# Optimization experiments

Hardware: AMD Instinct MI355X
Metric: run time of the kernel (lower is better)

Reference implementation:

```python
import jax, jax.numpy as jnp
import numpy as np

B, N, C = 8, 4096, 768
H = 4 * C  # mlp hidden
EPS = 1e-7
LN_EPS = 1e-5


def _ln(x, g, b):
    mu = jnp.mean(x, axis=-1, keepdims=True)
    var = jnp.mean((x - mu) ** 2, axis=-1, keepdims=True)
    return (x - mu) * jax.lax.rsqrt(var + LN_EPS) * g + b


def _mlp(z, w1, b1, w2, b2):
    return jax.nn.gelu(z @ w1 + b1, approximate=False) @ w2 + b2


def setup_inputs() -> dict:
    key = jax.random.key(0)
    ks = jax.random.split(key, 16)
    s = 1.0 / np.sqrt(C)
    inp = {
        "x": jax.random.normal(ks[0], (B, N, C), jnp.float32),
        "y": jax.random.normal(ks[1], (B, N, C), jnp.float32),
        "mask": jax.random.randint(ks[2], (B, N, 1), 0, 2).astype(jnp.float32),
        "h": 64,
        "w": 64,
        "ln1_g": jnp.ones((C,), jnp.float32),
        "ln1_b": jnp.zeros((C,), jnp.float32),
        "Wq": jax.random.normal(ks[3], (C, C), jnp.float32) * s,
        "Wk": jax.random.normal(ks[4], (C, C), jnp.float32) * s,
        "Wv": jax.random.normal(ks[5], (C, C), jnp.float32) * s,
        "Wpx": jax.random.normal(ks[6], (2 * C, C), jnp.float32) * s,
        "Wpy": jax.random.normal(ks[7], (2 * C, C), jnp.float32) * s,
        "ln2_g": jnp.ones((C,), jnp.float32),
        "ln2_b": jnp.zeros((C,), jnp.float32),
        "fx1_w": jax.random.normal(ks[8], (C, H), jnp.float32) * s,
        "fx1_b": jnp.zeros((H,), jnp.float32),
        "fx2_w": jax.random.normal(ks[9], (H, C), jnp.float32) / np.sqrt(H),
        "fx2_b": jnp.zeros((C,), jnp.float32),
        "fy1_w": jax.random.normal(ks[10], (C, H), jnp.float32) * s,
        "fy1_b": jnp.zeros((H,), jnp.float32),
        "fy2_w": jax.random.normal(ks[11], (H, C), jnp.float32) / np.sqrt(H),
        "fy2_b": jnp.zeros((C,), jnp.float32),
    }
    return inp


def _minmax(s):
    mn = jnp.min(s, axis=1, keepdims=True)
    mx = jnp.max(s, axis=1, keepdims=True)
    return (s - mn) / (mx - mn + EPS)


def reference(x, y, mask, h, w, ln1_g, ln1_b, Wq, Wk, Wv, Wpx, Wpy,
              ln2_g, ln2_b, fx1_w, fx1_b, fx2_w, fx2_b, fy1_w, fy1_b, fy2_w, fy2_b):
    b, n, c = x.shape
    m = mask.reshape(b, n, 1)  # binary mask per token
    xn = _ln(x, ln1_g, ln1_b)
    yn = _ln(y, ln1_g, ln1_b)
    q = yn @ Wq  # (b,n,c)
    k = xn @ Wk
    v = xn @ Wv
    # masked GAP pools (Weighted_GAP): (b,c)
    fg = jnp.sum(q * m, axis=1) / (jnp.sum(m, axis=1) + 5e-4)
    bg = jnp.sum(q * (1.0 - m), axis=1) / (jnp.sum(1.0 - m, axis=1) + 5e-4)
    k_nrm = jnp.linalg.norm(k, axis=2)  # (b,n)
    fg_nrm = jnp.linalg.norm(fg, axis=1, keepdims=True)  # (b,1)
    bg_nrm = jnp.linalg.norm(bg, axis=1, keepdims=True)
    fg_s = jnp.einsum('bnc,bc->bn', k, fg) / (k_nrm * fg_nrm + EPS)
    bg_s = jnp.einsum('bnc,bc->bn', k, bg) / (k_nrm * bg_nrm + EPS)
    scores = _minmax(fg_s) - _minmax(bg_s)  # (b,n)
    pseudo_mask = scores.reshape(b, 1, h, w)
    attn = jax.nn.softmax(jnp.where(scores < 0, scores - 100.0, scores), axis=1)
    query_pro = jnp.einsum('bn,bnc->bc', attn, v)  # (b,c)
    qp_nrm = jnp.linalg.norm(query_pro, axis=1, keepdims=True)
    sim = jnp.sum(query_pro * fg, axis=1, keepdims=True) / (qp_nrm * fg_nrm + EPS)
    sim = (sim + 1.0) * 0.5  # (b,1)
    pro = sim * fg + (1.0 - sim) * query_pro  # (b,c)
    pro_b = jnp.broadcast_to(pro[:, None, :], x.shape)
    xo = x + jnp.concatenate([x, pro_b], axis=-1) @ Wpx
    yo = y + jnp.concatenate([y, pro_b], axis=-1) @ Wpy
    xo = xo + _mlp(_ln(xo, ln2_g, ln2_b), fx1_w, fx1_b, fx2_w, fx2_b)
    yo = yo + _mlp(_ln(yo, ln2_g, ln2_b), fy1_w, fy1_b, fy2_w, fy2_b)
    return (xo, yo, pseudo_mask)
```

## Files before the change

### kernel.cpp

```cpp
#include <hip/hip_runtime.h>
#include <math.h>

#define B_ 8
#define N_ 4096
#define C_ 768
#define H_ 3072
#define M_ (B_*N_)
#define NSPLIT 16

typedef unsigned short u16;
typedef unsigned int u32;
typedef __attribute__((ext_vector_type(8))) __bf16 bf16x8;
typedef __attribute__((ext_vector_type(4))) float f32x4;
typedef __attribute__((ext_vector_type(4))) unsigned short u16x4;

__device__ __forceinline__ u16 f2bf(float f){
  u32 u = __float_as_uint(f);
  u32 r = (u + 0x7FFFu + ((u >> 16) & 1u)) >> 16;
  return (u16)r;
}
__device__ __forceinline__ float bf2f(u16 h){
  return __uint_as_float(((u32)h) << 16);
}
__device__ __forceinline__ void gload_lds16(const void* g, void* l){
  __builtin_amdgcn_global_load_lds((const __attribute__((address_space(1))) void*)g,
                                   (__attribute__((address_space(3))) void*)l, 16, 0, 0);
}

template<int EPI>
__global__ __launch_bounds__(256) void gemm_bf16(
    const u16* __restrict__ A, const u16* __restrict__ BT,
    int K, int N, int NBN,
    void* __restrict__ outp,
    const float* __restrict__ resid,
    const float* __restrict__ rowv,
    const float* __restrict__ bias)
{
  __shared__ u16 lds[2][8192];
  const int tid = threadIdx.x;
  const int wid = tid >> 6, lane = tid & 63;

  const int nwg = gridDim.x;
  int wg = blockIdx.x;
  wg = (wg & 7) * (nwg >> 3) + (wg >> 3);
  const int GMN = 8 * NBN;
  const int g = wg / GMN, r = wg % GMN;
  const int bm = (g*8 + (r & 7)) * 128;
  const int bn = (r >> 3) * 128;

  const int wr = wid >> 1, wc = wid & 1;

  f32x4 acc[4][4];
#pragma unroll
  for (int i=0;i<4;i++)
#pragma unroll
    for (int j=0;j<4;j++) acc[i][j] = (f32x4){0.f,0.f,0.f,0.f};

  const int idx0 = tid, idx1 = tid + 256;
  const u16* agp0 = A  + (size_t)(bm + (idx0>>2))*K + (idx0&3)*8;
  const u16* agp1 = A  + (size_t)(bm + (idx1>>2))*K + (idx1&3)*8;
  const u16* bgp0 = BT + (size_t)(bn + (idx0>>2))*K + (idx0&3)*8;
  const u16* bgp1 = BT + (size_t)(bn + (idx1>>2))*K + (idx1&3)*8;

  auto STAGE = [&](int c){
    u16* base = lds[c];
    gload_lds16(agp0, base + wid*512);
    gload_lds16(agp1, base + 2048 + wid*512);
    gload_lds16(bgp0, base + 4096 + wid*512);
    gload_lds16(bgp1, base + 6144 + wid*512);
    agp0 += 32; agp1 += 32; bgp0 += 32; bgp1 += 32;
  };

  const int aoff = (wr*64 + (lane&15))*32 + (lane>>4)*8;
  const int boff = 4096 + (wc*64 + (lane&15))*32 + (lane>>4)*8;

  const int nk = K >> 5;
  STAGE(0);
  __syncthreads();
  int cur = 0;
  for (int kk=0; kk<nk; kk++){
    if (kk+1 < nk) STAGE(cur^1);
    bf16x8 av[4], bv[4];
    const u16* pa = &lds[cur][aoff];
    const u16* pb = &lds[cur][boff];
#pragma unroll
    for (int i=0;i<4;i++){
      av[i] = *reinterpret_cast<const bf16x8*>(pa + i*512);
      bv[i] = *reinterpret_cast<const bf16x8*>(pb + i*512);
    }
#pragma unroll
    for (int i=0;i<4;i++)
#pragma unroll
      for (int j=0;j<4;j++)
        acc[i][j] = __builtin_amdgcn_mfma_f32_16x16x32_bf16(av[i], bv[j], acc[i][j], 0, 0, 0);
    __syncthreads();
    cur ^= 1;
  }

  const int col0 = bn + wc*64 + (lane & 15);
  const int row0 = bm + wr*64 + ((lane >> 4) << 2);
#pragma unroll
  for (int i=0;i<4;i++){
#pragma unroll
    for (int j=0;j<4;j++){
#pragma unroll
      for (int r2=0;r2<4;r2++){
        const int row = row0 + i*16 + r2;
        const int cj  = col0 + j*16;
        const size_t o = (size_t)row*N + cj;
        const float va = acc[i][j][r2];
        if constexpr (EPI == 0){
          ((u16*)outp)[o] = f2bf(va);
        } else if constexpr (EPI == 1){
          ((float*)outp)[o] = resid[o] + va + rowv[(row >> 12)*N + cj];
        } else if constexpr (EPI == 2){
          const float z = va + bias[cj];
          ((u16*)outp)[o] = f2bf(0.5f*z*(1.0f + erff(z*0.70710678f)));
        } else {
          float* po = (float*)outp + o;
          *po += va + bias[cj];
        }
      }
    }
  }
}

__global__ __launch_bounds__(256) void ln_fwd(const float* __restrict__ in,
    const float* __restrict__ gam, const float* __restrict__ bet,
    u16* __restrict__ out)
{
  const int row  = blockIdx.x*4 + (threadIdx.x >> 6);
  const int lane = threadIdx.x & 63;
  const float* p = in + (size_t)row * C_;
  float4 v0 = *reinterpret_cast<const float4*>(p + lane*4);
  float4 v1 = *reinterpret_cast<const float4*>(p + lane*4 + 256);
  float4 v2 = *reinterpret_cast<const float4*>(p + lane*4 + 512);
  float s  = v0.x+v0.y+v0.z+v0.w + v1.x+v1.y+v1.z+v1.w + v2.x+v2.y+v2.z+v2.w;
  float sq = v0.x*v0.x+v0.y*v0.y+v0.z*v0.z+v0.w*v0.w
           + v1.x*v1.x+v1.y*v1.y+v1.z*v1.z+v1.w*v1.w
           + v2.x*v2.x+v2.y*v2.y+v2.z*v2.z+v2.w*v2.w;
#pragma unroll
  for (int o=32;o>0;o>>=1){ s += __shfl_xor(s,o); sq += __shfl_xor(sq,o); }
  const float mu = s * (1.f/C_);
  const float rs = rsqrtf(sq*(1.f/C_) - mu*mu + 1e-5f);
  float4 g0 = *reinterpret_cast<const float4*>(gam + lane*4);
  float4 g1 = *reinterpret_cast<const float4*>(gam + lane*4 + 256);
  float4 g2 = *reinterpret_cast<const float4*>(gam + lane*4 + 512);
  float4 b0 = *reinterpret_cast<const float4*>(bet + lane*4);
  float4 b1 = *reinterpret_cast<const float4*>(bet + lane*4 + 256);
  float4 b2 = *reinterpret_cast<const float4*>(bet + lane*4 + 512);
  u16* op = out + (size_t)row * C_;
  u16x4 o0, o1, o2;
  o0[0]=f2bf((v0.x-mu)*rs*g0.x+b0.x); o0[1]=f2bf((v0.y-mu)*rs*g0.y+b0.y);
  o0[2]=f2bf((v0.z-mu)*rs*g0.z+b0.z); o0[3]=f2bf((v0.w-mu)*rs*g0.w+b0.w);
  o1[0]=f2bf((v1.x-mu)*rs*g1.x+b1.x); o1[1]=f2bf((v1.y-mu)*rs*g1.y+b1.y);
  o1[2]=f2bf((v1.z-mu)*rs*g1.z+b1.z); o1[3]=f2bf((v1.w-mu)*rs*g1.w+b1.w);
  o2[0]=f2bf((v2.x-mu)*rs*g2.x+b2.x); o2[1]=f2bf((v2.y-mu)*rs*g2.y+b2.y);
  o2[2]=f2bf((v2.z-mu)*rs*g2.z+b2.z); o2[3]=f2bf((v2.w-mu)*rs*g2.w+b2.w);
  *reinterpret_cast<u16x4*>(op + lane*4)       = o0;
  *reinterpret_cast<u16x4*>(op + lane*4 + 256) = o1;
  *reinterpret_cast<u16x4*>(op + lane*4 + 512) = o2;
}

__global__ __launch_bounds__(256) void cvt_bf16(const float* __restrict__ in,
                                                u16* __restrict__ out, int n4)
{
  int i = blockIdx.x*256 + threadIdx.x;
  if (i < n4){
    float4 v = reinterpret_cast<const float4*>(in)[i];
    u16x4 o; o[0]=f2bf(v.x); o[1]=f2bf(v.y); o[2]=f2bf(v.z); o[3]=f2bf(v.w);
    *reinterpret_cast<u16x4*>(out + (size_t)i*4) = o;
  }
}

__global__ __launch_bounds__(256) void transpose_cvt(const float* __restrict__ in,
    u16* __restrict__ out, int R, int Cc)
{
  __shared__ float tile[32][33];
  const int c0 = blockIdx.x*32, r0 = blockIdx.y*32;
  const int tx = threadIdx.x & 31, ty = threadIdx.x >> 5;
#pragma unroll
  for (int i=0;i<32;i+=8)
    tile[ty+i][tx] = in[(size_t)(r0+ty+i)*Cc + c0+tx];
  __syncthreads();
#pragma unroll
  for (int i=0;i<32;i+=8)
    out[(size_t)(c0+ty+i)*R + r0+tx] = f2bf(tile[tx][ty+i]);
}

__global__ __launch_bounds__(256) void msum_kernel(const float* __restrict__ mask,
                                                   float* __restrict__ msum)
{
  __shared__ float sm[4];
  const int b = blockIdx.x;
  float s = 0.f;
  for (int i=threadIdx.x;i<N_;i+=256) s += mask[(size_t)b*N_+i];
#pragma unroll
  for (int o=32;o>0;o>>=1) s += __shfl_down(s,o);
  if ((threadIdx.x&63)==0) sm[threadIdx.x>>6]=s;
  __syncthreads();
  if (threadIdx.x==0) msum[b] = sm[0]+sm[1]+sm[2]+sm[3];
}

__global__ __launch_bounds__(256) void pool_partial(const u16* __restrict__ q,
    const float* __restrict__ mask, float* __restrict__ pm, float* __restrict__ pa)
{
  const int c = blockIdx.x*256 + threadIdx.x;
  const int b = blockIdx.y, z = blockIdx.z;
  const int n0 = z*(N_/NSPLIT);
  const u16* qp = q + ((size_t)b*N_ + n0)*C_ + c;
  const float* mp = mask + (size_t)b*N_ + n0;
  float am=0.f, aa=0.f;
  for (int n=0;n<N_/NSPLIT;n++){
    float v = bf2f(qp[(size_t)n*C_]);
    float m = mp[n];
    am += v*m; aa += v;
  }
  const size_t o = ((size_t)z*B_ + b)*C_ + c;
  pm[o]=am; pa[o]=aa;
}

__global__ __launch_bounds__(256) void pool_final(const float* __restrict__ pm,
    const float* __restrict__ pa, const float* __restrict__ msum,
    float* __restrict__ fgin, float* __restrict__ bgin)
{
  const int c = blockIdx.x*256 + threadIdx.x;
  const int b = blockIdx.y;
  float s_m=0.f, s_a=0.f;
  for (int z=0;z<NSPLIT;z++){ size_t o=((size_t)z*B_+b)*C_+c; s_m+=pm[o]; s_a+=pa[o]; }
  const float ms = msum[b];
  fgin[b*C_+c] = s_m/(ms + 5e-4f);
  bgin[b*C_+c] = (s_a - s_m)/((float)N_ - ms + 5e-4f);
}

__global__ __launch_bounds__(256) void vecmat(const float* __restrict__ in,
    const float* __restrict__ W, int rowoff, float* __restrict__ outv)
{
  const int j = blockIdx.x*256 + threadIdx.x;
  const int b = blockIdx.y;
  const float* w = W + (size_t)rowoff*C_ + j;
  const float* p = in + b*C_;
  float acc=0.f;
#pragma unroll 4
  for (int c=0;c<C_;c++) acc += p[c]*w[(size_t)c*C_];
  outv[b*C_+j] = acc;
}

__global__ __launch_bounds__(256) void vecmat2(const float* __restrict__ in1,
    const float* __restrict__ in2, const float* __restrict__ W,
    float* __restrict__ o1, float* __restrict__ o2)
{
  const int j = blockIdx.x*256 + threadIdx.x;
  const int b = blockIdx.y;
  const float* w = W + j;
  const float* p1 = in1 + b*C_;
  const float* p2 = in2 + b*C_;
  float a1=0.f, a2=0.f;
#pragma unroll 4
  for (int c=0;c<C_;c++){ float wv = w[(size_t)c*C_]; a1 += p1[c]*wv; a2 += p2[c]*wv; }
  o1[b*C_+j]=a1; o2[b*C_+j]=a2;
}

__global__ __launch_bounds__(256) void norm_kernel(const float* __restrict__ fg,
    const float* __restrict__ bg, float* __restrict__ fgn, float* __restrict__ bgn)
{
  __shared__ float sm[8];
  const int b = blockIdx.x;
  float f=0.f, g=0.f;
  for (int i=threadIdx.x;i<C_;i+=256){
    float a=fg[b*C_+i]; f+=a*a;
    float c=bg[b*C_+i]; g+=c*c;
  }
#pragma unroll
  for (int o=32;o>0;o>>=1){ f+=__shfl_down(f,o); g+=__shfl_down(g,o); }
  if ((threadIdx.x&63)==0){ sm[threadIdx.x>>6]=f; sm[4+(threadIdx.x>>6)]=g; }
  __syncthreads();
  if (threadIdx.x==0){
    fgn[b]=sqrtf(sm[0]+sm[1]+sm[2]+sm[3]);
    bgn[b]=sqrtf(sm[4]+sm[5]+sm[6]+sm[7]);
  }
}

__global__ __launch_bounds__(256) void score_kernel(const u16* __restrict__ k,
    const float* __restrict__ fg, const float* __restrict__ bg,
    const float* __restrict__ fgn, const float* __restrict__ bgn,
    float* __restrict__ fg_s, float* __restrict__ bg_s)
{
  __shared__ float sm[12];
  const int t = blockIdx.x;
  const int b = t >> 12;
  const u16* kp = k + (size_t)t*C_;
  float df=0.f, db=0.f, kk=0.f;
  for (int i=threadIdx.x;i<C_;i+=256){
    float kv = bf2f(kp[i]);
    df += kv*fg[b*C_+i]; db += kv*bg[b*C_+i]; kk += kv*kv;
  }
#pragma unroll
  for (int o=32;o>0;o>>=1){ df+=__shfl_down(df,o); db+=__shfl_down(db,o); kk+=__shfl_down(kk,o); }
  const int wid = threadIdx.x>>6;
  if ((threadIdx.x&63)==0){ sm[wid]=df; sm[4+wid]=db; sm[8+wid]=kk; }
  __syncthreads();
  if (threadIdx.x==0){
    df=sm[0]+sm[1]+sm[2]+sm[3]; db=sm[4]+sm[5]+sm[6]+sm[7]; kk=sm[8]+sm[9]+sm[10]+sm[11];
    const float kn = sqrtf(kk);
    fg_s[t] = df/(kn*fgn[b]+1e-7f);
    bg_s[t] = db/(kn*bgn[b]+1e-7f);
  }
}

__global__ __launch_bounds__(256) void minmax_kernel(const float* __restrict__ fg_s,
    const float* __restrict__ bg_s, float* __restrict__ mm)
{
  __shared__ float sm[16];
  const int b = blockIdx.x;
  float mnf=1e30f, mxf=-1e30f, mnb=1e30f, mxb=-1e30f;
  for (int i=threadIdx.x;i<N_;i+=256){
    float a = fg_s[(size_t)b*N_+i]; mnf=fminf(mnf,a); mxf=fmaxf(mxf,a);
    float c = bg_s[(size_t)b*N_+i]; mnb=fminf(mnb,c); mxb=fmaxf(mxb,c);
  }
#pragma unroll
  for (int o=32;o>0;o>>=1){
    mnf=fminf(mnf,__shfl_down(mnf,o)); mxf=fmaxf(mxf,__shfl_down(mxf,o));
    mnb=fminf(mnb,__shfl_down(mnb,o)); mxb=fmaxf(mxb,__shfl_down(mxb,o));
  }
  const int wid = threadIdx.x>>6;
  if ((threadIdx.x&63)==0){ sm[wid]=mnf; sm[4+wid]=mxf; sm[8+wid]=mnb; sm[12+wid]=mxb; }
  __syncthreads();
  if (threadIdx.x==0){
    mm[b*4+0]=fminf(fminf(sm[0],sm[1]),fminf(sm[2],sm[3]));
    mm[b*4+1]=fmaxf(fmaxf(sm[4],sm[5]),fmaxf(sm[6],sm[7]));
    mm[b*4+2]=fminf(fminf(sm[8],sm[9]),fminf(sm[10],sm[11]));
    mm[b*4+3]=fmaxf(fmaxf(sm[12],sm[13]),fmaxf(sm[14],sm[15]));
  }
}

__global__ __launch_bounds__(256) void scorefin_kernel(const float* __restrict__ fg_s,
    const float* __restrict__ bg_s, const float* __restrict__ mm,
    float* __restrict__ pseudo, float* __restrict__ escr, float* __restrict__ epart)
{
  __shared__ float sm[4];
  const int b = blockIdx.y, z = blockIdx.x;
  const int t = z*256 + threadIdx.x;
  const size_t o = (size_t)b*N_ + t;
  const float mnf=mm[b*4+0], mxf=mm[b*4+1], mnb=mm[b*4+2], mxb=mm[b*4+3];
  const float s = (fg_s[o]-mnf)/(mxf-mnf+1e-7f) - (bg_s[o]-mnb)/(mxb-mnb+1e-7f);
  pseudo[o] = s;
  const float e = expf(s < 0.f ? s - 100.f : s);
  escr[o] = e;
  float ps = e;
#pragma unroll
  for (int off=32;off>0;off>>=1) ps += __shfl_down(ps,off);
  if ((threadIdx.x&63)==0) sm[threadIdx.x>>6]=ps;
  __syncthreads();
  if (threadIdx.x==0) epart[b*16+z] = sm[0]+sm[1]+sm[2]+sm[3];
}

__global__ void denom_kernel(const float* __restrict__ epart, float* __restrict__ denom){
  const int b = threadIdx.x;
  if (b < B_){ float s=0.f; for (int z=0;z<16;z++) s+=epart[b*16+z]; denom[b]=s; }
}

__global__ __launch_bounds__(256) void vpool_partial(const u16* __restrict__ xn,
    const float* __restrict__ e, float* __restrict__ pv)
{
  const int c = blockIdx.x*256 + threadIdx.x;
  const int b = blockIdx.y, z = blockIdx.z;
  const int n0 = z*(N_/NSPLIT);
  const u16* vp = xn + ((size_t)b*N_ + n0)*C_ + c;
  const float* ep = e + (size_t)b*N_ + n0;
  float acc=0.f;
  for (int n=0;n<N_/NSPLIT;n++) acc += bf2f(vp[(size_t)n*C_])*ep[n];
  pv[((size_t)z*B_+b)*C_+c] = acc;
}

__global__ __launch_bounds__(256) void vpool_final(const float* __restrict__ pv,
    const float* __restrict__ denom, float* __restrict__ vpin)
{
  const int c = blockIdx.x*256 + threadIdx.x;
  const int b = blockIdx.y;
  float s=0.f;
  for (int z=0;z<NSPLIT;z++) s += pv[((size_t)z*B_+b)*C_+c];
  vpin[b*C_+c] = s/denom[b];
}

__global__ __launch_bounds__(256) void pro_kernel(const float* __restrict__ qp,
    const float* __restrict__ fg, const float* __restrict__ fgn, float* __restrict__ pro)
{
  __shared__ float sm[8];
  __shared__ float simsh;
  const int b = blockIdx.x;
  float d=0.f, qq=0.f;
  for (int i=threadIdx.x;i<C_;i+=256){ float a=qp[b*C_+i]; d+=a*fg[b*C_+i]; qq+=a*a; }
#pragma unroll
  for (int o=32;o>0;o>>=1){ d+=__shfl_down(d,o); qq+=__shfl_down(qq,o); }
  if ((threadIdx.x&63)==0){ sm[threadIdx.x>>6]=d; sm[4+(threadIdx.x>>6)]=qq; }
  __syncthreads();
  if (threadIdx.x==0){
    d=sm[0]+sm[1]+sm[2]+sm[3]; qq=sm[4]+sm[5]+sm[6]+sm[7];
    simsh = (d/(sqrtf(qq)*fgn[b]+1e-7f)+1.f)*0.5f;
  }
  __syncthreads();
  const float sim = simsh;
  for (int i=threadIdx.x;i<C_;i+=256)
    pro[b*C_+i] = sim*fg[b*C_+i] + (1.f-sim)*qp[b*C_+i];
}

extern "C" void kernel_launch(void* const* d_in, const int* in_sizes, int n_in,
                              void* d_out, int out_size, void* d_ws, size_t ws_size,
                              hipStream_t stream)
{
  const float* x     = (const float*)d_in[0];
  const float* y     = (const float*)d_in[1];
  const float* mask  = (const float*)d_in[2];
  const float* ln1_g = (const float*)d_in[5];
  const float* ln1_b = (const float*)d_in[6];
  const float* Wq    = (const float*)d_in[7];
  const float* Wk    = (const float*)d_in[8];
  const float* Wv    = (const float*)d_in[9];
  const float* Wpx   = (const float*)d_in[10];
  const float* Wpy   = (const float*)d_in[11];
  const float* ln2_g = (const float*)d_in[12];
  const float* ln2_b = (const float*)d_in[13];
  const float* fx1_w = (const float*)d_in[14];
  const float* fx1_b = (const float*)d_in[15];
  const float* fx2_w = (const float*)d_in[16];
  const float* fx2_b = (const float*)d_in[17];
  const float* fy1_w = (const float*)d_in[18];
  const float* fy1_b = (const float*)d_in[19];
  const float* fy2_w = (const float*)d_in[20];
  const float* fy2_b = (const float*)d_in[21];

  float* out    = (float*)d_out;
  float* out_xo = out;
  float* out_yo = out + (size_t)M_*C_;
  float* out_ps = out + 2*(size_t)M_*C_;

  char* ws = (char*)d_ws;
  const size_t ACT = (size_t)M_*C_;
  u16* R0  = (u16*)ws;
  u16* xnb = R0;
  u16* ynb = R0 + ACT;
  u16* kb  = R0 + 2*ACT;
  u16* hid = R0;
  u16* qb  = (u16*)(ws + 4*ACT*2);
  u16* wp  = (u16*)(ws + 5*ACT*2);
  u16* WkT  = wp;
  u16* WpxT = wp + 1*589824;
  u16* WpyT = wp + 2*589824;
  u16* fx1T = wp + 3*589824;
  u16* fx2T = fx1T + 2359296;
  u16* fy1T = fx2T + 2359296;
  u16* fy2T = fy1T + 2359296;
  float* st   = (float*)(ws + 5*ACT*2 + (size_t)(3*589824 + 4*2359296)*2);
  float* msum = st;
  float* fgn  = st + 8;
  float* bgn  = st + 16;
  float* denom= st + 24;
  float* mm   = st + 32;
  float* fg   = st + 64;
  float* bg   = st + 6208;
  float* qp   = st + 12352;
  float* pro  = st + 18496;
  float* rowx = st + 24640;
  float* rowy = st + 30784;
  float* epart= st + 36928;
  float* fg_s = st + 37056;
  float* bg_s = st + 69824;
  float* escr = st + 102592;
  float* pm   = st + 135360;
  float* pa   = st + 233664;
  float* pv   = st + 331968;
  float* fgin = st + 430272;
  float* bgin = st + 436416;
  float* vpin = st + 442560;

  dim3 tb(256);

  transpose_cvt<<<dim3(24,24),tb,0,stream>>>(Wk,  WkT,  C_, C_);
  transpose_cvt<<<dim3(24,24),tb,0,stream>>>(Wpx, WpxT, C_, C_);
  transpose_cvt<<<dim3(24,24),tb,0,stream>>>(Wpy, WpyT, C_, C_);
  transpose_cvt<<<dim3(96,24),tb,0,stream>>>(fx1_w, fx1T, C_, H_);
  transpose_cvt<<<dim3(24,96),tb,0,stream>>>(fx2_w, fx2T, H_, C_);
  transpose_cvt<<<dim3(96,24),tb,0,stream>>>(fy1_w, fy1T, C_, H_);
  transpose_cvt<<<dim3(24,96),tb,0,stream>>>(fy2_w, fy2T, H_, C_);

  ln_fwd<<<M_/4,tb,0,stream>>>(x, ln1_g, ln1_b, xnb);
  ln_fwd<<<M_/4,tb,0,stream>>>(y, ln1_g, ln1_b, ynb);

  gemm_bf16<0><<<dim3(256*6),tb,0,stream>>>(xnb, WkT, C_, C_, 6, kb, nullptr,nullptr,nullptr);

  msum_kernel<<<B_,tb,0,stream>>>(mask, msum);
  pool_partial<<<dim3(3,B_,NSPLIT),tb,0,stream>>>(ynb, mask, pm, pa);
  pool_final<<<dim3(3,B_),tb,0,stream>>>(pm, pa, msum, fgin, bgin);
  vecmat2<<<dim3(3,B_),tb,0,stream>>>(fgin, bgin, Wq, fg, bg);
  norm_kernel<<<B_,tb,0,stream>>>(fg, bg, fgn, bgn);

  score_kernel<<<M_,tb,0,stream>>>(kb, fg, bg, fgn, bgn, fg_s, bg_s);
  minmax_kernel<<<B_,tb,0,stream>>>(fg_s, bg_s, mm);
  scorefin_kernel<<<dim3(16,B_),tb,0,stream>>>(fg_s, bg_s, mm, out_ps, escr, epart);
  denom_kernel<<<1,64,0,stream>>>(epart, denom);

  vpool_partial<<<dim3(3,B_,NSPLIT),tb,0,stream>>>(xnb, escr, pv);
  vpool_final<<<dim3(3,B_),tb,0,stream>>>(pv, denom, vpin);
  vecmat<<<dim3(3,B_),tb,0,stream>>>(vpin, Wv, 0, qp);

  pro_kernel<<<B_,tb,0,stream>>>(qp, fg, fgn, pro);
  vecmat<<<dim3(3,B_),tb,0,stream>>>(pro, Wpx, C_, rowx);
  vecmat<<<dim3(3,B_),tb,0,stream>>>(pro, Wpy, C_, rowy);

  cvt_bf16<<<(ACT/4+255)/256,tb,0,stream>>>(x, xnb, (int)(ACT/4));
  cvt_bf16<<<(ACT/4+255)/256,tb,0,stream>>>(y, ynb, (int)(ACT/4));

  gemm_bf16<1><<<dim3(256*6),tb,0,stream>>>(xnb, WpxT, C_, C_, 6, out_xo, x, rowx, nullptr);
  gemm_bf16<1><<<dim3(256*6),tb,0,stream>>>(ynb, WpyT, C_, C_, 6, out_yo, y, rowy, nullptr);

  ln_fwd<<<M_/4,tb,0,stream>>>(out_xo, ln2_g, ln2_b, qb);
  gemm_bf16<2><<<dim3(256*24),tb,0,stream>>>(qb, fx1T, C_, H_, 24, hid, nullptr,nullptr, fx1_b);
  gemm_bf16<3><<<dim3(256*6),tb,0,stream>>>(hid, fx2T, H_, C_, 6, out_xo, nullptr,nullptr, fx2_b);

  ln_fwd<<<M_/4,tb,0,stream>>>(out_yo, ln2_g, ln2_b, qb);
  gemm_bf16<2><<<dim3(256*24),tb,0,stream>>>(qb, fy1T, C_, H_, 24, hid, nullptr,nullptr, fy1_b);
  gemm_bf16<3><<<dim3(256*6),tb,0,stream>>>(hid, fy2T, H_, C_, 6, out_yo, nullptr,nullptr, fy2_b);
}
```

Before: 1.866 ms.

## Enlarge GEMM tiles to 256x128 with 512 threads and fuse small prototype kernels

The GEMM now runs 8 waves per block on a 256x128 output tile, sharing each B tile across two M halves, and uses a larger LDS buffer. Many small launches are merged: the seven weight transposes, the two layer norms, the two conversions, the mask sum with the pooling, the pool finish with the Wq product and norms, the score finish with the denominator, and the value pool finish with the Wv/Wpx/Wpy products. The score kernel now handles one row per wave with vector loads. This cuts launch count and redundant memory traffic and raises GEMM data reuse, at the cost of more LDS per block and a few serial 8-block kernels doing larger matrix-vector loops.

```diff
diff --git a/kernel.cpp b/kernel.cpp
--- a/kernel.cpp
+++ b/kernel.cpp
@@ -13,6 +13,7 @@
 typedef __attribute__((ext_vector_type(8))) __bf16 bf16x8;
 typedef __attribute__((ext_vector_type(4))) float f32x4;
 typedef __attribute__((ext_vector_type(4))) unsigned short u16x4;
+typedef __attribute__((ext_vector_type(8))) unsigned short u16x8;
 
 __device__ __forceinline__ u16 f2bf(float f){
   u32 u = __float_as_uint(f);
@@ -28,7 +29,7 @@
 }
 
 template<int EPI>
-__global__ __launch_bounds__(256) void gemm_bf16(
+__global__ __launch_bounds__(512, 4) void gemm_bf16(
     const u16* __restrict__ A, const u16* __restrict__ BT,
     int K, int N, int NBN,
     void* __restrict__ outp,
@@ -36,7 +37,7 @@
     const float* __restrict__ rowv,
     const float* __restrict__ bias)
 {
-  __shared__ u16 lds[2][8192];
+  __shared__ u16 lds[2][12288];
   const int tid = threadIdx.x;
   const int wid = tid >> 6, lane = tid & 63;
 
@@ -45,7 +46,7 @@
   wg = (wg & 7) * (nwg >> 3) + (wg >> 3);
   const int GMN = 8 * NBN;
   const int g = wg / GMN, r = wg % GMN;
-  const int bm = (g*8 + (r & 7)) * 128;
+  const int bm = (g*8 + (r & 7)) * 256;
   const int bn = (r >> 3) * 128;
 
   const int wr = wid >> 1, wc = wid & 1;
@@ -56,23 +57,20 @@
 #pragma unroll
     for (int j=0;j<4;j++) acc[i][j] = (f32x4){0.f,0.f,0.f,0.f};
 
-  const int idx0 = tid, idx1 = tid + 256;
-  const u16* agp0 = A  + (size_t)(bm + (idx0>>2))*K + (idx0&3)*8;
-  const u16* agp1 = A  + (size_t)(bm + (idx1>>2))*K + (idx1&3)*8;
-  const u16* bgp0 = BT + (size_t)(bn + (idx0>>2))*K + (idx0&3)*8;
-  const u16* bgp1 = BT + (size_t)(bn + (idx1>>2))*K + (idx1&3)*8;
+  const u16* agp0 = A  + (size_t)(bm + (tid>>2))*K + (tid&3)*8;
+  const u16* agp1 = A  + (size_t)(bm + 128 + (tid>>2))*K + (tid&3)*8;
+  const u16* bgp0 = BT + (size_t)(bn + (tid>>2))*K + (tid&3)*8;
 
   auto STAGE = [&](int c){
-    u16* base = lds[c];
-    gload_lds16(agp0, base + wid*512);
-    gload_lds16(agp1, base + 2048 + wid*512);
-    gload_lds16(bgp0, base + 4096 + wid*512);
-    gload_lds16(bgp1, base + 6144 + wid*512);
-    agp0 += 32; agp1 += 32; bgp0 += 32; bgp1 += 32;
+    char* base = (char*)lds[c] + wid*1024;
+    gload_lds16(agp0, base);
+    gload_lds16(agp1, base + 8192);
+    gload_lds16(bgp0, base + 16384);
+    agp0 += 32; agp1 += 32; bgp0 += 32;
   };
 
-  const int aoff = (wr*64 + (lane&15))*32 + (lane>>4)*8;
-  const int boff = 4096 + (wc*64 + (lane&15))*32 + (lane>>4)*8;
+  const int aoff = (wr*64 + (lane&15))*32 + ((lane>>4)<<3);
+  const int boff = 8192 + (wc*64 + (lane&15))*32 + ((lane>>4)<<3);
 
   const int nk = K >> 5;
   STAGE(0);
@@ -125,13 +123,10 @@
   }
 }
 
-__global__ __launch_bounds__(256) void ln_fwd(const float* __restrict__ in,
+__device__ __forceinline__ void ln_row(const float* __restrict__ p,
     const float* __restrict__ gam, const float* __restrict__ bet,
-    u16* __restrict__ out)
-{
-  const int row  = blockIdx.x*4 + (threadIdx.x >> 6);
-  const int lane = threadIdx.x & 63;
-  const float* p = in + (size_t)row * C_;
+    u16* __restrict__ op, int lane)
+{
   float4 v0 = *reinterpret_cast<const float4*>(p + lane*4);
   float4 v1 = *reinterpret_cast<const float4*>(p + lane*4 + 256);
   float4 v2 = *reinterpret_cast<const float4*>(p + lane*4 + 512);
@@ -149,7 +144,6 @@
   float4 b0 = *reinterpret_cast<const float4*>(bet + lane*4);
   float4 b1 = *reinterpret_cast<const float4*>(bet + lane*4 + 256);
   float4 b2 = *reinterpret_cast<const float4*>(bet + lane*4 + 512);
-  u16* op = out + (size_t)row * C_;
   u16x4 o0, o1, o2;
   o0[0]=f2bf((v0.x-mu)*rs*g0.x+b0.x); o0[1]=f2bf((v0.y-mu)*rs*g0.y+b0.y);
   o0[2]=f2bf((v0.z-mu)*rs*g0.z+b0.z); o0[3]=f2bf((v0.w-mu)*rs*g0.w+b0.w);
@@ -162,10 +156,33 @@
   *reinterpret_cast<u16x4*>(op + lane*4 + 512) = o2;
 }
 
-__global__ __launch_bounds__(256) void cvt_bf16(const float* __restrict__ in,
-                                                u16* __restrict__ out, int n4)
+__global__ __launch_bounds__(256) void ln_fwd(const float* __restrict__ in,
+    const float* __restrict__ gam, const float* __restrict__ bet,
+    u16* __restrict__ out)
+{
+  const int row  = blockIdx.x*4 + (threadIdx.x >> 6);
+  const int lane = threadIdx.x & 63;
+  ln_row(in + (size_t)row*C_, gam, bet, out + (size_t)row*C_, lane);
+}
+
+__global__ __launch_bounds__(256) void ln_fwd2(const float* __restrict__ inx,
+    const float* __restrict__ iny, const float* __restrict__ gam,
+    const float* __restrict__ bet, u16* __restrict__ outx, u16* __restrict__ outy)
+{
+  const int row  = blockIdx.x*4 + (threadIdx.x >> 6);
+  const int lane = threadIdx.x & 63;
+  const float* in = blockIdx.y ? iny : inx;
+  u16* out = blockIdx.y ? outy : outx;
+  ln_row(in + (size_t)row*C_, gam, bet, out + (size_t)row*C_, lane);
+}
+
+__global__ __launch_bounds__(256) void cvt2_bf16(const float* __restrict__ inx,
+    const float* __restrict__ iny, u16* __restrict__ outx, u16* __restrict__ outy,
+    int n4)
 {
   int i = blockIdx.x*256 + threadIdx.x;
+  const float* in = blockIdx.y ? iny : inx;
+  u16* out = blockIdx.y ? outy : outx;
   if (i < n4){
     float4 v = reinterpret_cast<const float4*>(in)[i];
     u16x4 o; o[0]=f2bf(v.x); o[1]=f2bf(v.y); o[2]=f2bf(v.z); o[3]=f2bf(v.w);
@@ -173,11 +190,12 @@
   }
 }
 
-__global__ __launch_bounds__(256) void transpose_cvt(const float* __restrict__ in,
-    u16* __restrict__ out, int R, int Cc)
+__device__ __forceinline__ void tr_tile(const float* __restrict__ in,
+    u16* __restrict__ outp, int R, int Cc, int t)
 {
   __shared__ float tile[32][33];
-  const int c0 = blockIdx.x*32, r0 = blockIdx.y*32;
+  const int tilesx = Cc >> 5;
+  const int c0 = (t % tilesx)*32, r0 = (t / tilesx)*32;
   const int tx = threadIdx.x & 31, ty = threadIdx.x >> 5;
 #pragma unroll
   for (int i=0;i<32;i+=8)
@@ -185,99 +203,89 @@
   __syncthreads();
 #pragma unroll
   for (int i=0;i<32;i+=8)
-    out[(size_t)(c0+ty+i)*R + r0+tx] = f2bf(tile[tx][ty+i]);
-}
-
-__global__ __launch_bounds__(256) void msum_kernel(const float* __restrict__ mask,
-                                                   float* __restrict__ msum)
-{
-  __shared__ float sm[4];
-  const int b = blockIdx.x;
-  float s = 0.f;
-  for (int i=threadIdx.x;i<N_;i+=256) s += mask[(size_t)b*N_+i];
-#pragma unroll
-  for (int o=32;o>0;o>>=1) s += __shfl_down(s,o);
-  if ((threadIdx.x&63)==0) sm[threadIdx.x>>6]=s;
-  __syncthreads();
-  if (threadIdx.x==0) msum[b] = sm[0]+sm[1]+sm[2]+sm[3];
+    outp[(size_t)(c0+ty+i)*R + r0+tx] = f2bf(tile[tx][ty+i]);
+}
+
+__global__ __launch_bounds__(256) void transpose_all(
+    const float* Wk, const float* Wpx, const float* Wpy,
+    const float* f1x, const float* f2x, const float* f1y, const float* f2y,
+    u16* WkT, u16* WpxT, u16* WpyT, u16* f1xT, u16* f2xT, u16* f1yT, u16* f2yT)
+{
+  int t = blockIdx.x;
+  if (t < 1728){
+    const int m = t / 576; t -= m*576;
+    const float* in = (m==0)?Wk:((m==1)?Wpx:Wpy);
+    u16* o = (m==0)?WkT:((m==1)?WpxT:WpyT);
+    tr_tile(in, o, C_, C_, t);
+  } else {
+    t -= 1728;
+    const int m = t / 2304; t -= m*2304;
+    if (m==0)      tr_tile(f1x, f1xT, C_, H_, t);
+    else if (m==1) tr_tile(f2x, f2xT, H_, C_, t);
+    else if (m==2) tr_tile(f1y, f1yT, C_, H_, t);
+    else           tr_tile(f2y, f2yT, H_, C_, t);
+  }
 }
 
 __global__ __launch_bounds__(256) void pool_partial(const u16* __restrict__ q,
-    const float* __restrict__ mask, float* __restrict__ pm, float* __restrict__ pa)
+    const float* __restrict__ mask, float* __restrict__ pm, float* __restrict__ pa,
+    float* __restrict__ mpart)
 {
   const int c = blockIdx.x*256 + threadIdx.x;
   const int b = blockIdx.y, z = blockIdx.z;
   const int n0 = z*(N_/NSPLIT);
   const u16* qp = q + ((size_t)b*N_ + n0)*C_ + c;
   const float* mp = mask + (size_t)b*N_ + n0;
-  float am=0.f, aa=0.f;
+  float am=0.f, aa=0.f, ms=0.f;
   for (int n=0;n<N_/NSPLIT;n++){
     float v = bf2f(qp[(size_t)n*C_]);
     float m = mp[n];
-    am += v*m; aa += v;
+    am += v*m; aa += v; ms += m;
   }
   const size_t o = ((size_t)z*B_ + b)*C_ + c;
   pm[o]=am; pa[o]=aa;
-}
-
-__global__ __launch_bounds__(256) void pool_final(const float* __restrict__ pm,
-    const float* __restrict__ pa, const float* __restrict__ msum,
-    float* __restrict__ fgin, float* __restrict__ bgin)
-{
-  const int c = blockIdx.x*256 + threadIdx.x;
-  const int b = blockIdx.y;
-  float s_m=0.f, s_a=0.f;
-  for (int z=0;z<NSPLIT;z++){ size_t o=((size_t)z*B_+b)*C_+c; s_m+=pm[o]; s_a+=pa[o]; }
-  const float ms = msum[b];
-  fgin[b*C_+c] = s_m/(ms + 5e-4f);
-  bgin[b*C_+c] = (s_a - s_m)/((float)N_ - ms + 5e-4f);
-}
-
-__global__ __launch_bounds__(256) void vecmat(const float* __restrict__ in,
-    const float* __restrict__ W, int rowoff, float* __restrict__ outv)
-{
-  const int j = blockIdx.x*256 + threadIdx.x;
-  const int b = blockIdx.y;
-  const float* w = W + (size_t)rowoff*C_ + j;
-  const float* p = in + b*C_;
-  float acc=0.f;
-#pragma unroll 4
-  for (int c=0;c<C_;c++) acc += p[c]*w[(size_t)c*C_];
-  outv[b*C_+j] = acc;
-}
-
-__global__ __launch_bounds__(256) void vecmat2(const float* __restrict__ in1,
-    const float* __restrict__ in2, const float* __restrict__ W,
-    float* __restrict__ o1, float* __restrict__ o2)
-{
-  const int j = blockIdx.x*256 + threadIdx.x;
-  const int b = blockIdx.y;
-  const float* w = W + j;
-  const float* p1 = in1 + b*C_;
-  const float* p2 = in2 + b*C_;
-  float a1=0.f, a2=0.f;
-#pragma unroll 4
-  for (int c=0;c<C_;c++){ float wv = w[(size_t)c*C_]; a1 += p1[c]*wv; a2 += p2[c]*wv; }
-  o1[b*C_+j]=a1; o2[b*C_+j]=a2;
-}
-
-__global__ __launch_bounds__(256) void norm_kernel(const float* __restrict__ fg,
-    const float* __restrict__ bg, float* __restrict__ fgn, float* __restrict__ bgn)
-{
-  __shared__ float sm[8];
-  const int b = blockIdx.x;
-  float f=0.f, g=0.f;
-  for (int i=threadIdx.x;i<C_;i+=256){
-    float a=fg[b*C_+i]; f+=a*a;
-    float c=bg[b*C_+i]; g+=c*c;
-  }
-#pragma unroll
-  for (int o=32;o>0;o>>=1){ f+=__shfl_down(f,o); g+=__shfl_down(g,o); }
-  if ((threadIdx.x&63)==0){ sm[threadIdx.x>>6]=f; sm[4+(threadIdx.x>>6)]=g; }
-  __syncthreads();
-  if (threadIdx.x==0){
-    fgn[b]=sqrtf(sm[0]+sm[1]+sm[2]+sm[3]);
-    bgn[b]=sqrtf(sm[4]+sm[5]+sm[6]+sm[7]);
+  if (blockIdx.x==0 && threadIdx.x==0) mpart[z*B_+b] = ms;
+}
+
+__global__ __launch_bounds__(256) void proto_fused(const float* __restrict__ pm,
+    const float* __restrict__ pa, const float* __restrict__ mpart,
+    const float* __restrict__ Wq,
+    float* __restrict__ fg, float* __restrict__ bg,
+    float* __restrict__ fgn, float* __restrict__ bgn)
+{
+  __shared__ float fin[C_], bin[C_];
+  __shared__ float red[8];
+  const int b = blockIdx.x, tid = threadIdx.x;
+  float msum_b = 0.f;
+#pragma unroll
+  for (int z=0;z<NSPLIT;z++) msum_b += mpart[z*B_+b];
+  for (int c=tid;c<C_;c+=256){
+    float sm=0.f, sa=0.f;
+#pragma unroll
+    for (int z=0;z<NSPLIT;z++){ size_t o=((size_t)z*B_+b)*C_+c; sm+=pm[o]; sa+=pa[o]; }
+    fin[c] = sm/(msum_b + 5e-4f);
+    bin[c] = (sa - sm)/((float)N_ - msum_b + 5e-4f);
+  }
+  __syncthreads();
+  const int j0 = tid, j1 = tid+256, j2 = tid+512;
+  float f0=0,f1=0,f2=0,g0=0,g1=0,g2=0;
+  for (int c=0;c<C_;c++){
+    const float* w = Wq + (size_t)c*C_;
+    float fc = fin[c], bc = bin[c];
+    float w0=w[j0], w1=w[j1], w2=w[j2];
+    f0 += fc*w0; f1 += fc*w1; f2 += fc*w2;
+    g0 += bc*w0; g1 += bc*w1; g2 += bc*w2;
+  }
+  fg[b*C_+j0]=f0; fg[b*C_+j1]=f1; fg[b*C_+j2]=f2;
+  bg[b*C_+j0]=g0; bg[b*C_+j1]=g1; bg[b*C_+j2]=g2;
+  float sf = f0*f0+f1*f1+f2*f2, sb = g0*g0+g1*g1+g2*g2;
+#pragma unroll
+  for (int o=32;o>0;o>>=1){ sf+=__shfl_down(sf,o); sb+=__shfl_down(sb,o); }
+  if ((tid&63)==0){ red[tid>>6]=sf; red[4+(tid>>6)]=sb; }
+  __syncthreads();
+  if (tid==0){
+    fgn[b]=sqrtf(red[0]+red[1]+red[2]+red[3]);
+    bgn[b]=sqrtf(red[4]+red[5]+red[6]+red[7]);
   }
 }
 
@@ -286,22 +294,39 @@
     const float* __restrict__ fgn, const float* __restrict__ bgn,
     float* __restrict__ fg_s, float* __restrict__ bg_s)
 {
-  __shared__ float sm[12];
-  const int t = blockIdx.x;
+  const int t = blockIdx.x*4 + (threadIdx.x >> 6);
+  const int lane = threadIdx.x & 63;
   const int b = t >> 12;
   const u16* kp = k + (size_t)t*C_;
-  float df=0.f, db=0.f, kk=0.f;
-  for (int i=threadIdx.x;i<C_;i+=256){
-    float kv = bf2f(kp[i]);
-    df += kv*fg[b*C_+i]; db += kv*bg[b*C_+i]; kk += kv*kv;
-  }
-#pragma unroll
-  for (int o=32;o>0;o>>=1){ df+=__shfl_down(df,o); db+=__shfl_down(db,o); kk+=__shfl_down(kk,o); }
-  const int wid = threadIdx.x>>6;
-  if ((threadIdx.x&63)==0){ sm[wid]=df; sm[4+wid]=db; sm[8+wid]=kk; }
-  __syncthreads();
-  if (threadIdx.x==0){
-    df=sm[0]+sm[1]+sm[2]+sm[3]; db=sm[4]+sm[5]+sm[6]+sm[7]; kk=sm[8]+sm[9]+sm[10]+sm[11];
+  u16x8 k8 = *reinterpret_cast<const u16x8*>(kp + lane*8);
+  u16x4 k4 = *reinterpret_cast<const u16x4*>(kp + 512 + lane*4);
+  const float* fgp = fg + b*C_;
+  const float* bgp = bg + b*C_;
+  float4 fa = *reinterpret_cast<const float4*>(fgp + lane*8);
+  float4 fb = *reinterpret_cast<const float4*>(fgp + lane*8 + 4);
+  float4 fc = *reinterpret_cast<const float4*>(fgp + 512 + lane*4);
+  float4 ba = *reinterpret_cast<const float4*>(bgp + lane*8);
+  float4 bb = *reinterpret_cast<const float4*>(bgp + lane*8 + 4);
+  float4 bc = *reinterpret_cast<const float4*>(bgp + 512 + lane*4);
+  float kv[12];
+#pragma unroll
+  for (int i=0;i<8;i++) kv[i] = bf2f(k8[i]);
+#pragma unroll
+  for (int i=0;i<4;i++) kv[8+i] = bf2f(k4[i]);
+  float df = kv[0]*fa.x+kv[1]*fa.y+kv[2]*fa.z+kv[3]*fa.w
+           + kv[4]*fb.x+kv[5]*fb.y+kv[6]*fb.z+kv[7]*fb.w
+           + kv[8]*fc.x+kv[9]*fc.y+kv[10]*fc.z+kv[11]*fc.w;
+  float db = kv[0]*ba.x+kv[1]*ba.y+kv[2]*ba.z+kv[3]*ba.w
+           + kv[4]*bb.x+kv[5]*bb.y+kv[6]*bb.z+kv[7]*bb.w
+           + kv[8]*bc.x+kv[9]*bc.y+kv[10]*bc.z+kv[11]*bc.w;
+  float kk=0.f;
+#pragma unroll
+  for (int i=0;i<12;i++) kk += kv[i]*kv[i];
+#pragma unroll
+  for (int o=32;o>0;o>>=1){
+    df+=__shfl_xor(df,o); db+=__shfl_xor(db,o); kk+=__shfl_xor(kk,o);
+  }
+  if (lane==0){
     const float kn = sqrtf(kk);
     fg_s[t] = df/(kn*fgn[b]+1e-7f);
     bg_s[t] = db/(kn*bgn[b]+1e-7f);
@@ -334,30 +359,35 @@
   }
 }
 
-__global__ __launch_bounds__(256) void scorefin_kernel(const float* __restrict__ fg_s,
+__global__ __launch_bounds__(1024) void scorefin_fused(const float* __restrict__ fg_s,
     const float* __restrict__ bg_s, const float* __restrict__ mm,
-    float* __restrict__ pseudo, float* __restrict__ escr, float* __restrict__ epart)
-{
-  __shared__ float sm[4];
-  const int b = blockIdx.y, z = blockIdx.x;
-  const int t = z*256 + threadIdx.x;
-  const size_t o = (size_t)b*N_ + t;
+    float* __restrict__ pseudo, float* __restrict__ escr, float* __restrict__ denom)
+{
+  __shared__ float sm[16];
+  const int b = blockIdx.x, tid = threadIdx.x;
   const float mnf=mm[b*4+0], mxf=mm[b*4+1], mnb=mm[b*4+2], mxb=mm[b*4+3];
-  const float s = (fg_s[o]-mnf)/(mxf-mnf+1e-7f) - (bg_s[o]-mnb)/(mxb-mnb+1e-7f);
-  pseudo[o] = s;
-  const float e = expf(s < 0.f ? s - 100.f : s);
-  escr[o] = e;
-  float ps = e;
-#pragma unroll
-  for (int off=32;off>0;off>>=1) ps += __shfl_down(ps,off);
-  if ((threadIdx.x&63)==0) sm[threadIdx.x>>6]=ps;
-  __syncthreads();
-  if (threadIdx.x==0) epart[b*16+z] = sm[0]+sm[1]+sm[2]+sm[3];
-}
-
-__global__ void denom_kernel(const float* __restrict__ epart, float* __restrict__ denom){
-  const int b = threadIdx.x;
-  if (b < B_){ float s=0.f; for (int z=0;z<16;z++) s+=epart[b*16+z]; denom[b]=s; }
+  const float rf = 1.f/(mxf-mnf+1e-7f), rb = 1.f/(mxb-mnb+1e-7f);
+  float ps = 0.f;
+#pragma unroll
+  for (int i=0;i<4;i++){
+    const int t = tid + i*1024;
+    const size_t o = (size_t)b*N_ + t;
+    const float s = (fg_s[o]-mnf)*rf - (bg_s[o]-mnb)*rb;
+    pseudo[o] = s;
+    const float e = expf(s < 0.f ? s - 100.f : s);
+    escr[o] = e;
+    ps += e;
+  }
+#pragma unroll
+  for (int o=32;o>0;o>>=1) ps += __shfl_down(ps,o);
+  if ((tid&63)==0) sm[tid>>6]=ps;
+  __syncthreads();
+  if (tid==0){
+    float s=0.f;
+#pragma unroll
+    for (int w=0;w<16;w++) s+=sm[w];
+    denom[b]=s;
+  }
 }
 
 __global__ __launch_bounds__(256) void vpool_partial(const u16* __restrict__ xn,
@@ -373,36 +403,59 @@
   pv[((size_t)z*B_+b)*C_+c] = acc;
 }
 
-__global__ __launch_bounds__(256) void vpool_final(const float* __restrict__ pv,
-    const float* __restrict__ denom, float* __restrict__ vpin)
-{
-  const int c = blockIdx.x*256 + threadIdx.x;
-  const int b = blockIdx.y;
-  float s=0.f;
-  for (int z=0;z<NSPLIT;z++) s += pv[((size_t)z*B_+b)*C_+c];
-  vpin[b*C_+c] = s/denom[b];
-}
-
-__global__ __launch_bounds__(256) void pro_kernel(const float* __restrict__ qp,
-    const float* __restrict__ fg, const float* __restrict__ fgn, float* __restrict__ pro)
-{
-  __shared__ float sm[8];
+__global__ __launch_bounds__(256) void pro_fused(const float* __restrict__ pv,
+    const float* __restrict__ denom,
+    const float* __restrict__ Wv, const float* __restrict__ Wpx,
+    const float* __restrict__ Wpy,
+    const float* __restrict__ fg, const float* __restrict__ fgn,
+    float* __restrict__ rowx, float* __restrict__ rowy)
+{
+  __shared__ float vin[C_];
+  __shared__ float red[8];
   __shared__ float simsh;
-  const int b = blockIdx.x;
-  float d=0.f, qq=0.f;
-  for (int i=threadIdx.x;i<C_;i+=256){ float a=qp[b*C_+i]; d+=a*fg[b*C_+i]; qq+=a*a; }
+  const int b = blockIdx.x, tid = threadIdx.x;
+  const float den = 1.f/denom[b];
+  for (int c=tid;c<C_;c+=256){
+    float s=0.f;
+#pragma unroll
+    for (int z=0;z<NSPLIT;z++) s += pv[((size_t)z*B_+b)*C_+c];
+    vin[c] = s*den;
+  }
+  __syncthreads();
+  const int j0 = tid, j1 = tid+256, j2 = tid+512;
+  float q0=0,q1=0,q2=0;
+  for (int c=0;c<C_;c++){
+    const float* w = Wv + (size_t)c*C_;
+    float vv = vin[c];
+    q0 += vv*w[j0]; q1 += vv*w[j1]; q2 += vv*w[j2];
+  }
+  const float fg0 = fg[b*C_+j0], fg1 = fg[b*C_+j1], fg2 = fg[b*C_+j2];
+  float d = q0*fg0 + q1*fg1 + q2*fg2;
+  float qq = q0*q0 + q1*q1 + q2*q2;
 #pragma unroll
   for (int o=32;o>0;o>>=1){ d+=__shfl_down(d,o); qq+=__shfl_down(qq,o); }
-  if ((threadIdx.x&63)==0){ sm[threadIdx.x>>6]=d; sm[4+(threadIdx.x>>6)]=qq; }
-  __syncthreads();
-  if (threadIdx.x==0){
-    d=sm[0]+sm[1]+sm[2]+sm[3]; qq=sm[4]+sm[5]+sm[6]+sm[7];
-    simsh = (d/(sqrtf(qq)*fgn[b]+1e-7f)+1.f)*0.5f;
+  if ((tid&63)==0){ red[tid>>6]=d; red[4+(tid>>6)]=qq; }
+  __syncthreads();
+  if (tid==0){
+    float dd=red[0]+red[1]+red[2]+red[3], qs=red[4]+red[5]+red[6]+red[7];
+    simsh = (dd/(sqrtf(qs)*fgn[b]+1e-7f)+1.f)*0.5f;
   }
   __syncthreads();
   const float sim = simsh;
-  for (int i=threadIdx.x;i<C_;i+=256)
-    pro[b*C_+i] = sim*fg[b*C_+i] + (1.f-sim)*qp[b*C_+i];
+  vin[j0] = sim*fg0 + (1.f-sim)*q0;
+  vin[j1] = sim*fg1 + (1.f-sim)*q1;
+  vin[j2] = sim*fg2 + (1.f-sim)*q2;
+  __syncthreads();
+  float rx0=0,rx1=0,rx2=0, ry0=0,ry1=0,ry2=0;
+  for (int c=0;c<C_;c++){
+    const float* wx = Wpx + (size_t)(C_+c)*C_;
+    const float* wy = Wpy + (size_t)(C_+c)*C_;
+    float pc = vin[c];
+    rx0 += pc*wx[j0]; rx1 += pc*wx[j1]; rx2 += pc*wx[j2];
+    ry0 += pc*wy[j0]; ry1 += pc*wy[j1]; ry2 += pc*wy[j2];
+  }
+  rowx[b*C_+j0]=rx0; rowx[b*C_+j1]=rx1; rowx[b*C_+j2]=rx2;
+  rowy[b*C_+j0]=ry0; rowy[b*C_+j1]=ry1; rowy[b*C_+j2]=ry2;
 }
 
 extern "C" void kernel_launch(void* const* d_in, const int* in_sizes, int n_in,
@@ -452,73 +505,51 @@
   u16* fy1T = fx2T + 2359296;
   u16* fy2T = fy1T + 2359296;
   float* st   = (float*)(ws + 5*ACT*2 + (size_t)(3*589824 + 4*2359296)*2);
-  float* msum = st;
   float* fgn  = st + 8;
   float* bgn  = st + 16;
   float* denom= st + 24;
   float* mm   = st + 32;
   float* fg   = st + 64;
   float* bg   = st + 6208;
-  float* qp   = st + 12352;
-  float* pro  = st + 18496;
   float* rowx = st + 24640;
   float* rowy = st + 30784;
-  float* epart= st + 36928;
   float* fg_s = st + 37056;
   float* bg_s = st + 69824;
   float* escr = st + 102592;
   float* pm   = st + 135360;
   float* pa   = st + 233664;
   float* pv   = st + 331968;
-  float* fgin = st + 430272;
-  float* bgin = st + 436416;
-  float* vpin = st + 442560;
+  float* mpart= st + 430272;
 
   dim3 tb(256);
-
-  transpose_cvt<<<dim3(24,24),tb,0,stream>>>(Wk,  WkT,  C_, C_);
-  transpose_cvt<<<dim3(24,24),tb,0,stream>>>(Wpx, WpxT, C_, C_);
-  transpose_cvt<<<dim3(24,24),tb,0,stream>>>(Wpy, WpyT, C_, C_);
-  transpose_cvt<<<dim3(96,24),tb,0,stream>>>(fx1_w, fx1T, C_, H_);
-  transpose_cvt<<<dim3(24,96),tb,0,stream>>>(fx2_w, fx2T, H_, C_);
-  transpose_cvt<<<dim3(96,24),tb,0,stream>>>(fy1_w, fy1T, C_, H_);
-  transpose_cvt<<<dim3(24,96),tb,0,stream>>>(fy2_w, fy2T, H_, C_);
-
-  ln_fwd<<<M_/4,tb,0,stream>>>(x, ln1_g, ln1_b, xnb);
-  ln_fwd<<<M_/4,tb,0,stream>>>(y, ln1_g, ln1_b, ynb);
-
-  gemm_bf16<0><<<dim3(256*6),tb,0,stream>>>(xnb, WkT, C_, C_, 6, kb, nullptr,nullptr,nullptr);
-
-  msum_kernel<<<B_,tb,0,stream>>>(mask, msum);
-  pool_partial<<<dim3(3,B_,NSPLIT),tb,0,stream>>>(ynb, mask, pm, pa);
-  pool_final<<<dim3(3,B_),tb,0,stream>>>(pm, pa, msum, fgin, bgin);
-  vecmat2<<<dim3(3,B_),tb,0,stream>>>(fgin, bgin, Wq, fg, bg);
-  norm_kernel<<<B_,tb,0,stream>>>(fg, bg, fgn, bgn);
-
-  score_kernel<<<M_,tb,0,stream>>>(kb, fg, bg, fgn, bgn, fg_s, bg_s);
+  dim3 tg(512);
+
+  transpose_all<<<dim3(10944),tb,0,stream>>>(Wk,Wpx,Wpy,fx1_w,fx2_w,fy1_w,fy2_w,
+                                             WkT,WpxT,WpyT,fx1T,fx2T,fy1T,fy2T);
+  ln_fwd2<<<dim3(M_/4,2),tb,0,stream>>>(x, y, ln1_g, ln1_b, xnb, ynb);
+
+  gemm_bf16<0><<<dim3(128*6),tg,0,stream>>>(xnb, WkT, C_, C_, 6, kb, nullptr,nullptr,nullptr);
+
+  pool_partial<<<dim3(3,B_,NSPLIT),tb,0,stream>>>(ynb, mask, pm, pa, mpart);
+  proto_fused<<<B_,tb,0,stream>>>(pm, pa, mpart, Wq, fg, bg, fgn, bgn);
+
+  score_kernel<<<M_/4,tb,0,stream>>>(kb, fg, bg, fgn, bgn, fg_s, bg_s);
   minmax_kernel<<<B_,tb,0,stream>>>(fg_s, bg_s, mm);
-  scorefin_kernel<<<dim3(16,B_),tb,0,stream>>>(fg_s, bg_s, mm, out_ps, escr, epart);
-  denom_kernel<<<1,64,0,stream>>>(epart, denom);
+  scorefin_fused<<<B_,dim3(1024),0,stream>>>(fg_s, bg_s, mm, out_ps, escr, denom);
 
   vpool_partial<<<dim3(3,B_,NSPLIT),tb,0,stream>>>(xnb, escr, pv);
-  vpool_final<<<dim3(3,B_),tb,0,stream>>>(pv, denom, vpin);
-  vecmat<<<dim3(3,B_),tb,0,stream>>>(vpin, Wv, 0, qp);
-
-  pro_kernel<<<B_,tb,0,stream>>>(qp, fg, fgn, pro);
-  vecmat<<<dim3(3,B_),tb,0,stream>>>(pro, Wpx, C_, rowx);
-  vecmat<<<dim3(3,B_),tb,0,stream>>>(pro, Wpy, C_, rowy);
-
-  cvt_bf16<<<(ACT/4+255)/256,tb,0,stream>>>(x, xnb, (int)(ACT/4));
-  cvt_bf16<<<(ACT/4+255)/256,tb,0,stream>>>(y, ynb, (int)(ACT/4));
-
-  gemm_bf16<1><<<dim3(256*6),tb,0,stream>>>(xnb, WpxT, C_, C_, 6, out_xo, x, rowx, nullptr);
-  gemm_bf16<1><<<dim3(256*6),tb,0,stream>>>(ynb, WpyT, C_, C_, 6, out_yo, y, rowy, nullptr);
+  pro_fused<<<B_,tb,0,stream>>>(pv, denom, Wv, Wpx, Wpy, fg, fgn, rowx, rowy);
+
+  cvt2_bf16<<<dim3((ACT/4+255)/256,2),tb,0,stream>>>(x, y, xnb, ynb, (int)(ACT/4));
+
+  gemm_bf16<1><<<dim3(128*6),tg,0,stream>>>(xnb, WpxT, C_, C_, 6, out_xo, x, rowx, nullptr);
+  gemm_bf16<1><<<dim3(128*6),tg,0,stream>>>(ynb, WpyT, C_, C_, 6, out_yo, y, rowy, nullptr);
 
   ln_fwd<<<M_/4,tb,0,stream>>>(out_xo, ln2_g, ln2_b, qb);
-  gemm_bf16<2><<<dim3(256*24),tb,0,stream>>>(qb, fx1T, C_, H_, 24, hid, nullptr,nullptr, fx1_b);
-  gemm_bf16<3><<<dim3(256*6),tb,0,stream>>>(hid, fx2T, H_, C_, 6, out_xo, nullptr,nullptr, fx2_b);
+  gemm_bf16<2><<<dim3(128*24),tg,0,stream>>>(qb, fx1T, C_, H_, 24, hid, nullptr,nullptr, fx1_b);
+  gemm_bf16<3><<<dim3(128*6),tg,0,stream>>>(hid, fx2T, H_, C_, 6, out_xo, nullptr,nullptr, fx2_b);
 
   ln_fwd<<<M_/4,tb,0,stream>>>(out_yo, ln2_g, ln2_b, qb);
-  gemm_bf16<2><<<dim3(256*24),tb,0,stream>>>(qb, fy1T, C_, H_, 24, hid, nullptr,nullptr, fy1_b);
-  gemm_bf16<3><<<dim3(256*6),tb,0,stream>>>(hid, fy2T, H_, C_, 6, out_yo, nullptr,nullptr, fy2_b);
-}
+  gemm_bf16<2><<<dim3(128*24),tg,0,stream>>>(qb, fy1T, C_, H_, 24, hid, nullptr,nullptr, fy1_b);
+  gemm_bf16<3><<<dim3(128*6),tg,0,stream>>>(hid, fy2T, H_, C_, 6, out_yo, nullptr,nullptr, fy2_b);
+}
```

New measurement: 1.621 ms. 1.15x faster.
